# Kernel optimization log

Measured on AMD Instinct MI355X. Metric: run time of the kernel, lower is better.

## Reference

```python
import jax, jax.numpy as jnp
import numpy as np

B, N, F_IN, F_OUT = 8, 2048, 64, 64
NEG = -9.0e15  # matches torch's -9000000000000000.0 mask value


def setup_inputs() -> dict:
    key = jax.random.key(0)
    ks = jax.random.split(key, 12)
    stdv1 = 1.0 / np.sqrt(F_IN)
    stdv2 = 1.0 / np.sqrt(2 * F_OUT)
    x = jax.random.normal(ks[0], (B, N, F_IN), dtype=jnp.float32)
    adj = jax.random.randint(ks[1], (B, N, N), 0, 2).astype(jnp.int32)
    identity = jnp.broadcast_to(jnp.eye(N, dtype=jnp.int32), (B, N, N))
    def unif(k, shape, s):
        return jax.random.uniform(k, shape, jnp.float32, -s, s)
    return {
        "x": x, "adj": adj, "identity": identity,
        "W1": unif(ks[2], (F_OUT, F_IN), stdv1), "b1": unif(ks[3], (F_OUT,), stdv1),
        "a1": unif(ks[4], (1, 2 * F_OUT), stdv2), "ab1": unif(ks[5], (1,), stdv2),
        "W2": unif(ks[6], (F_OUT, F_IN), stdv1), "b2": unif(ks[7], (F_OUT,), stdv1),
        "a2": unif(ks[8], (1, 2 * F_OUT), stdv2), "ab2": unif(ks[9], (1,), stdv2),
    }


def _gat_layer(x, mask, W, b, a, ab):
    # linear1
    h = jnp.einsum('bnf,of->bno', x, W) + b                     # [B,N,Fo]
    Fo = h.shape[-1]
    # linear2 on concat(h_i, h_j) decomposes: e_ij = relu(h_i.a1 + h_j.a2 + ab)
    s1 = h @ a[0, :Fo]                                          # [B,N]
    s2 = h @ a[0, Fo:]                                          # [B,N]
    e = jax.nn.relu(s1[:, :, None] + s2[:, None, :] + ab[0])    # [B,N,N]
    e = jnp.where(mask > 0, e, NEG)
    att = jax.nn.softmax(e, axis=2)                             # [B,N,N]
    return jnp.einsum('bnm,bmf->bnf', att, h)                   # dropout p=0 / eval


def reference(x, adj, identity, W1, b1, a1, ab1, W2, b2, a2, ab2):
    out1 = _gat_layer(x, adj, W1, b1, a1, ab1)
    out2 = _gat_layer(x, identity, W2, b2, a2, ab2)
    return out1 + out2
```

## Files before the change

### kernel.cpp

```cpp
#include <hip/hip_runtime.h>


#define DEVI __device__ __forceinline__

typedef __attribute__((ext_vector_type(8))) short short8;
typedef __attribute__((ext_vector_type(4))) float floatx4;

DEVI unsigned short f2bf(float x) {
    unsigned u = __builtin_bit_cast(unsigned, x);
    unsigned r = u + 0x7FFFu + ((u >> 16) & 1u);
    return (unsigned short)(r >> 16);
}

DEVI short8 pack8(const float* v) {
    short8 r;
#pragma unroll
    for (int i = 0; i < 8; ++i) r[i] = (short)f2bf(v[i]);
    return r;
}

DEVI unsigned cvt_pk_bf16(float lo, float hi) {
    unsigned r;
    asm("v_cvt_pk_bf16_f32 %0, %1, %2" : "=v"(r) : "v"(lo), "v"(hi));
    return r;
}

DEVI void team_sync() {
    __builtin_amdgcn_sched_barrier(0);
    asm volatile("s_waitcnt lgkmcnt(0)" ::: "memory");
    __builtin_amdgcn_s_barrier();
    __builtin_amdgcn_sched_barrier(0);
}

__global__ __launch_bounds__(256) void k_prep(
    const float* __restrict__ x, const float* __restrict__ W1,
    const float* __restrict__ b1, const float* __restrict__ a1,
    const float* __restrict__ ab1,
    unsigned short* __restrict__ hT1,
    float* __restrict__ expt1,
    float* __restrict__ expv)
{
    __shared__ __align__(16) unsigned short hstage[64][72];
    const int tid = threadIdx.x;
    const int w = tid >> 6, lane = tid & 63;
    const int g = lane >> 4, r15 = lane & 15;
    const int blockRow = blockIdx.x * 64;
    const int rowbase = blockRow + w * 16;

    float xa[8], xb[8];
    const float* xrow = x + (long)(rowbase + r15) * 64;
#pragma unroll
    for (int e = 0; e < 8; ++e) { xa[e] = xrow[g * 8 + e]; xb[e] = xrow[32 + g * 8 + e]; }
    short8 A0 = pack8(xa), A1 = pack8(xb);

    floatx4 acc[4];
#pragma unroll
    for (int nt = 0; nt < 4; ++nt) {
        float wa[8], wb[8];
        const float* wrow = W1 + (nt * 16 + r15) * 64;
#pragma unroll
        for (int e = 0; e < 8; ++e) { wa[e] = wrow[g * 8 + e]; wb[e] = wrow[32 + g * 8 + e]; }
        short8 B0 = pack8(wa), B1 = pack8(wb);
        floatx4 c = {0.f, 0.f, 0.f, 0.f};
        c = __builtin_amdgcn_mfma_f32_16x16x32_bf16(A0, B0, c, 0, 0, 0);
        c = __builtin_amdgcn_mfma_f32_16x16x32_bf16(A1, B1, c, 0, 0, 0);
        float bias = b1[nt * 16 + r15];
#pragma unroll
        for (int q = 0; q < 4; ++q) c[q] += bias;
        acc[nt] = c;
    }

    float a1lo[4], a1hi[4];
#pragma unroll
    for (int nt = 0; nt < 4; ++nt) {
        a1lo[nt] = a1[nt * 16 + r15];
        a1hi[nt] = a1[64 + nt * 16 + r15];
    }
    float s1q[4], s2q[4];
#pragma unroll
    for (int q = 0; q < 4; ++q) {
        float s1 = 0.f, s2 = 0.f;
#pragma unroll
        for (int nt = 0; nt < 4; ++nt) { s1 += acc[nt][q] * a1lo[nt]; s2 += acc[nt][q] * a1hi[nt]; }
#pragma unroll
        for (int m = 1; m < 16; m <<= 1) { s1 += __shfl_xor(s1, m); s2 += __shfl_xor(s2, m); }
        s1q[q] = s1; s2q[q] = s2;
    }
    if (r15 == 0) {
        float abv = ab1[0];
#pragma unroll
        for (int q = 0; q < 4; ++q) {
            expt1[rowbase + 4 * g + q] = __expf(s1q[q] + abv);
            expv[rowbase + 4 * g + q]  = __expf(s2q[q]);
        }
    }

#pragma unroll
    for (int nt = 0; nt < 4; ++nt)
#pragma unroll
        for (int q = 0; q < 4; ++q)
            hstage[nt * 16 + r15][w * 16 + 4 * g + q] = f2bf(acc[nt][q]);
    __syncthreads();
    {
        const int o = tid >> 2, seg = (tid & 3) * 16;
        const int bb = blockRow >> 11;
        const int ib = blockRow & 2047;
        unsigned short* dst = hT1 + ((long)(bb * 64 + o) * 2048) + ib + seg;
        uint4 v0 = *(const uint4*)&hstage[o][seg];
        uint4 v1 = *(const uint4*)&hstage[o][seg + 8];
        *(uint4*)dst = v0;
        *(uint4*)(dst + 8) = v1;
    }
}

__global__ __launch_bounds__(1024, 4) void k_attn(
    const float* __restrict__ x, const int* __restrict__ adj,
    const float* __restrict__ W2, const float* __restrict__ b2,
    const unsigned short* __restrict__ hT1,
    const float* __restrict__ expt1, const float* __restrict__ expv,
    float* __restrict__ out)
{
    __shared__ __align__(16) unsigned short hl[4][2][64][72];
    __shared__ __align__(16) float vlds[2048];

    const int tid = threadIdx.x;
    const int w = tid >> 6, lane = tid & 63;
    const int t = w >> 2, wrow = w & 3;
    const int g = lane >> 4, r15 = lane & 15;
    const int bb = blockIdx.x & 7;
    const int it = blockIdx.x >> 3;
    const int rowbase = it * 64 + wrow * 16;
    const int jt0 = t * 8;

    *(float2*)&vlds[tid * 2] = *(const float2*)&expv[bb * 2048 + tid * 2];

    const float u = expt1[bb * 2048 + rowbase + r15];

    floatx4 acc[4];
#pragma unroll
    for (int nt = 0; nt < 4; ++nt) acc[nt] = (floatx4){0.f, 0.f, 0.f, 0.f};
    floatx4 acc5 = {0.f, 0.f, 0.f, 0.f};

    short8 ones;
#pragma unroll
    for (int i = 0; i < 8; ++i) ones[i] = (short)0x3F80;

    const int4* adjq = (const int4*)(adj + (long)(bb * 2048 + rowbase + r15) * 2048);

    const int ttid = tid & 255;
    const int so = ttid >> 2, sseg = (ttid & 3) * 16;
    const unsigned short* hTsrc = hT1 + (long)(bb * 64 + so) * 2048 + sseg;
    unsigned short* hldst0 = &hl[t][0][so][sseg];
    unsigned short* hldst1 = &hl[t][1][so][sseg];

    int4 adjR[2][4];
    uint4 hrg[2][2];

#define ADJ(c) do {                                                            \
        const int base_ = (jt0 + (c)) * 16 + g * 2;                            \
        adjR[(c) & 1][0] = adjq[base_];                                        \
        adjR[(c) & 1][1] = adjq[base_ + 1];                                    \
        adjR[(c) & 1][2] = adjq[base_ + 8];                                    \
        adjR[(c) & 1][3] = adjq[base_ + 9];                                    \
    } while (0)

#define HTLOAD(c) do {                                                         \
        const unsigned short* s_ = hTsrc + (jt0 + (c)) * 64;                   \
        hrg[(c) & 1][0] = *(const uint4*)s_;                                   \
        hrg[(c) & 1][1] = *(const uint4*)(s_ + 8);                             \
    } while (0)

#define HTSTORE(c) do {                                                        \
        unsigned short* d_ = ((c) & 1) ? hldst1 : hldst0;                      \
        *(uint4*)d_ = hrg[(c) & 1][0];                                         \
        *(uint4*)(d_ + 8) = hrg[(c) & 1][1];                                   \
    } while (0)

#define COMPUTE(C) do {                                                        \
        const int vb_ = (jt0 + (C)) * 64 + g * 8;                              \
        float4 v0_ = *(const float4*)&vlds[vb_];                               \
        float4 v1_ = *(const float4*)&vlds[vb_ + 4];                           \
        float4 v2_ = *(const float4*)&vlds[vb_ + 32];                          \
        float4 v3_ = *(const float4*)&vlds[vb_ + 36];                          \
        int4 j0_ = adjR[(C) & 1][0], j1_ = adjR[(C) & 1][1];                   \
        int4 j2_ = adjR[(C) & 1][2], j3_ = adjR[(C) & 1][3];                   \
        uint4 au_, bu_;                                                        \
        au_.x = cvt_pk_bf16(j0_.x > 0 ? fmaxf(u * v0_.x, 1.f) : 0.f,           \
                            j0_.y > 0 ? fmaxf(u * v0_.y, 1.f) : 0.f);          \
        au_.y = cvt_pk_bf16(j0_.z > 0 ? fmaxf(u * v0_.z, 1.f) : 0.f,           \
                            j0_.w > 0 ? fmaxf(u * v0_.w, 1.f) : 0.f);          \
        au_.z = cvt_pk_bf16(j1_.x > 0 ? fmaxf(u * v1_.x, 1.f) : 0.f,           \
                            j1_.y > 0 ? fmaxf(u * v1_.y, 1.f) : 0.f);          \
        au_.w = cvt_pk_bf16(j1_.z > 0 ? fmaxf(u * v1_.z, 1.f) : 0.f,           \
                            j1_.w > 0 ? fmaxf(u * v1_.w, 1.f) : 0.f);          \
        bu_.x = cvt_pk_bf16(j2_.x > 0 ? fmaxf(u * v2_.x, 1.f) : 0.f,           \
                            j2_.y > 0 ? fmaxf(u * v2_.y, 1.f) : 0.f);          \
        bu_.y = cvt_pk_bf16(j2_.z > 0 ? fmaxf(u * v2_.z, 1.f) : 0.f,           \
                            j2_.w > 0 ? fmaxf(u * v2_.w, 1.f) : 0.f);          \
        bu_.z = cvt_pk_bf16(j3_.x > 0 ? fmaxf(u * v3_.x, 1.f) : 0.f,           \
                            j3_.y > 0 ? fmaxf(u * v3_.y, 1.f) : 0.f);          \
        bu_.w = cvt_pk_bf16(j3_.z > 0 ? fmaxf(u * v3_.z, 1.f) : 0.f,           \
                            j3_.w > 0 ? fmaxf(u * v3_.w, 1.f) : 0.f);          \
        short8 a0 = __builtin_bit_cast(short8, au_);                           \
        short8 a1 = __builtin_bit_cast(short8, bu_);                           \
        _Pragma("unroll")                                                      \
        for (int nt_ = 0; nt_ < 4; ++nt_) {                                    \
            short8 b0 = *(const short8*)&hl[t][(C) & 1][nt_ * 16 + r15][g * 8];      \
            short8 b1 = *(const short8*)&hl[t][(C) & 1][nt_ * 16 + r15][32 + g * 8]; \
            acc[nt_] = __builtin_amdgcn_mfma_f32_16x16x32_bf16(a0, b0, acc[nt_], 0, 0, 0); \
            acc[nt_] = __builtin_amdgcn_mfma_f32_16x16x32_bf16(a1, b1, acc[nt_], 0, 0, 0); \
        }                                                                      \
        acc5 = __builtin_amdgcn_mfma_f32_16x16x32_bf16(a0, ones, acc5, 0, 0, 0); \
        acc5 = __builtin_amdgcn_mfma_f32_16x16x32_bf16(a1, ones, acc5, 0, 0, 0); \
    } while (0)

    ADJ(0); ADJ(1);
    HTLOAD(0);
    HTSTORE(0);
    HTLOAD(1);
    team_sync();

#pragma unroll
    for (int C = 0; C < 8; ++C) {
        if (C < 6) HTLOAD(C + 2);
        if (C < 7) HTSTORE(C + 1);
        COMPUTE(C);
        if (C < 6) ADJ(C + 2);
        team_sync();
    }

#undef COMPUTE
#undef HTSTORE
#undef HTLOAD
#undef ADJ

    float* csh = (float*)&hl[0][0][0][0];
    if (t > 0) {
        const int wb = ((t - 1) * 4 + wrow) * 20;
#pragma unroll
        for (int nt = 0; nt < 4; ++nt)
#pragma unroll
            for (int q = 0; q < 4; ++q)
                csh[(wb + nt * 4 + q) * 64 + lane] = acc[nt][q];
#pragma unroll
        for (int q = 0; q < 4; ++q)
            csh[(wb + 16 + q) * 64 + lane] = acc5[q];
    }
    __syncthreads();

    if (t == 0) {
#pragma unroll
        for (int ti = 0; ti < 3; ++ti) {
            const int wb = (ti * 4 + wrow) * 20;
#pragma unroll
            for (int nt = 0; nt < 4; ++nt)
#pragma unroll
                for (int q = 0; q < 4; ++q)
                    acc[nt][q] += csh[(wb + nt * 4 + q) * 64 + lane];
#pragma unroll
            for (int q = 0; q < 4; ++q)
                acc5[q] += csh[(wb + 16 + q) * 64 + lane];
        }
        float linv[4];
#pragma unroll
        for (int q = 0; q < 4; ++q) linv[q] = 1.0f / acc5[q];

        float xa[8], xb[8];
        const float* xrow = x + ((long)(bb * 2048 + rowbase + r15)) * 64;
#pragma unroll
        for (int e = 0; e < 8; ++e) { xa[e] = xrow[g * 8 + e]; xb[e] = xrow[32 + g * 8 + e]; }
        short8 A0 = pack8(xa), A1 = pack8(xb);
#pragma unroll
        for (int nt = 0; nt < 4; ++nt) {
            float wa[8], wb[8];
            const float* wrow2 = W2 + (nt * 16 + r15) * 64;
#pragma unroll
            for (int e = 0; e < 8; ++e) { wa[e] = wrow2[g * 8 + e]; wb[e] = wrow2[32 + g * 8 + e]; }
            short8 B0 = pack8(wa), B1 = pack8(wb);
            floatx4 c = {0.f, 0.f, 0.f, 0.f};
            c = __builtin_amdgcn_mfma_f32_16x16x32_bf16(A0, B0, c, 0, 0, 0);
            c = __builtin_amdgcn_mfma_f32_16x16x32_bf16(A1, B1, c, 0, 0, 0);
            float bias = b2[nt * 16 + r15];
#pragma unroll
            for (int q = 0; q < 4; ++q) {
                float val = acc[nt][q] * linv[q] + c[q] + bias;
                out[((long)(bb * 2048 + rowbase + 4 * g + q)) * 64 + nt * 16 + r15] = val;
            }
        }
    }
}

extern "C" void kernel_launch(void* const* d_in, const int* in_sizes, int n_in,
                              void* d_out, int out_size, void* d_ws, size_t ws_size,
                              hipStream_t stream) {
    const float* x   = (const float*)d_in[0];
    const int*   adj = (const int*)d_in[1];
    const float* W1  = (const float*)d_in[3];
    const float* b1  = (const float*)d_in[4];
    const float* a1  = (const float*)d_in[5];
    const float* ab1 = (const float*)d_in[6];
    const float* W2  = (const float*)d_in[7];
    const float* b2  = (const float*)d_in[8];

    unsigned short* hT1 = (unsigned short*)d_ws;
    float* expt1 = (float*)((char*)d_ws + (size_t)8 * 64 * 2048 * 2);
    float* expv  = expt1 + 8 * 2048;

    k_prep<<<256, 256, 0, stream>>>(x, W1, b1, a1, ab1, hT1, expt1, expv);
    k_attn<<<256, 1024, 0, stream>>>(x, adj, W2, b2, hT1, expt1, expv, (float*)d_out);
}
```

Before: 39.61 us.

## Halve attention block size, XOR-swizzle the hT LDS tile, and reorder staging

Each attention block now has 512 threads in four 2-wave teams, covering 32 rows. This doubles the grid to 512 blocks. The padded 72-wide LDS tile for hT is replaced by an unpadded 64-wide tile with an XOR swizzle on 16-byte chunks, to avoid bank conflicts without the padding. Global-to-register staging of hT drops from two register buffers to one: each chunk is loaded before compute and written to LDS after it. This trades some prefetch depth for fewer registers and finer work distribution, and it depends on team_sync matching the new 2-wave team size.

```diff
diff --git a/kernel.cpp b/kernel.cpp
--- a/kernel.cpp
+++ b/kernel.cpp
@@ -113,26 +113,26 @@
     }
 }
 
-__global__ __launch_bounds__(1024, 4) void k_attn(
+__global__ __launch_bounds__(512, 4) void k_attn(
     const float* __restrict__ x, const int* __restrict__ adj,
     const float* __restrict__ W2, const float* __restrict__ b2,
     const unsigned short* __restrict__ hT1,
     const float* __restrict__ expt1, const float* __restrict__ expv,
     float* __restrict__ out)
 {
-    __shared__ __align__(16) unsigned short hl[4][2][64][72];
+    __shared__ __align__(16) unsigned short hl[4][2][64][64];
     __shared__ __align__(16) float vlds[2048];
 
     const int tid = threadIdx.x;
     const int w = tid >> 6, lane = tid & 63;
-    const int t = w >> 2, wrow = w & 3;
+    const int t = w >> 1, wrow = w & 1;
     const int g = lane >> 4, r15 = lane & 15;
     const int bb = blockIdx.x & 7;
     const int it = blockIdx.x >> 3;
-    const int rowbase = it * 64 + wrow * 16;
+    const int rowbase = it * 32 + wrow * 16;
     const int jt0 = t * 8;
 
-    *(float2*)&vlds[tid * 2] = *(const float2*)&expv[bb * 2048 + tid * 2];
+    *(float4*)&vlds[tid * 4] = *(const float4*)&expv[bb * 2048 + tid * 4];
 
     const float u = expt1[bb * 2048 + rowbase + r15];
 
@@ -147,14 +147,13 @@
 
     const int4* adjq = (const int4*)(adj + (long)(bb * 2048 + rowbase + r15) * 2048);
 
-    const int ttid = tid & 255;
-    const int so = ttid >> 2, sseg = (ttid & 3) * 16;
-    const unsigned short* hTsrc = hT1 + (long)(bb * 64 + so) * 2048 + sseg;
-    unsigned short* hldst0 = &hl[t][0][so][sseg];
-    unsigned short* hldst1 = &hl[t][1][so][sseg];
+    const int ttid = tid & 127;
+    const int so = ttid >> 1, ch = ttid & 1;
+    const unsigned short* hTsrc = hT1 + (long)(bb * 64 + so) * 2048 + ch * 32;
+    unsigned short* hlw = &hl[t][0][0][0];
 
     int4 adjR[2][4];
-    uint4 hrg[2][2];
+    uint4 hrg[4];
 
 #define ADJ(c) do {                                                            \
         const int base_ = (jt0 + (c)) * 16 + g * 2;                            \
@@ -166,14 +165,17 @@
 
 #define HTLOAD(c) do {                                                         \
         const unsigned short* s_ = hTsrc + (jt0 + (c)) * 64;                   \
-        hrg[(c) & 1][0] = *(const uint4*)s_;                                   \
-        hrg[(c) & 1][1] = *(const uint4*)(s_ + 8);                             \
+        hrg[0] = *(const uint4*)s_;                                            \
+        hrg[1] = *(const uint4*)(s_ + 8);                                      \
+        hrg[2] = *(const uint4*)(s_ + 16);                                     \
+        hrg[3] = *(const uint4*)(s_ + 24);                                     \
     } while (0)
 
 #define HTSTORE(c) do {                                                        \
-        unsigned short* d_ = ((c) & 1) ? hldst1 : hldst0;                      \
-        *(uint4*)d_ = hrg[(c) & 1][0];                                         \
-        *(uint4*)(d_ + 8) = hrg[(c) & 1][1];                                   \
+        const int bo_ = ((c) & 1) * 4096 + so * 64;                            \
+        _Pragma("unroll")                                                      \
+        for (int k_ = 0; k_ < 4; ++k_)                                         \
+            *(uint4*)&hlw[bo_ + (((ch * 4 + k_) ^ (so & 7)) * 8)] = hrg[k_];   \
     } while (0)
 
 #define COMPUTE(C) do {                                                        \
@@ -203,10 +205,13 @@
                             j3_.w > 0 ? fmaxf(u * v3_.w, 1.f) : 0.f);          \
         short8 a0 = __builtin_bit_cast(short8, au_);                           \
         short8 a1 = __builtin_bit_cast(short8, bu_);                           \
+        const int bufo_ = ((C) & 1) * 4096;                                    \
+        const int sw_ = r15 & 7;                                               \
         _Pragma("unroll")                                                      \
         for (int nt_ = 0; nt_ < 4; ++nt_) {                                    \
-            short8 b0 = *(const short8*)&hl[t][(C) & 1][nt_ * 16 + r15][g * 8];      \
-            short8 b1 = *(const short8*)&hl[t][(C) & 1][nt_ * 16 + r15][32 + g * 8]; \
+            const int ro_ = bufo_ + (nt_ * 16 + r15) * 64;                     \
+            short8 b0 = *(const short8*)&hlw[ro_ + ((g ^ sw_) * 8)];           \
+            short8 b1 = *(const short8*)&hlw[ro_ + (((4 + g) ^ sw_) * 8)];     \
             acc[nt_] = __builtin_amdgcn_mfma_f32_16x16x32_bf16(a0, b0, acc[nt_], 0, 0, 0); \
             acc[nt_] = __builtin_amdgcn_mfma_f32_16x16x32_bf16(a1, b1, acc[nt_], 0, 0, 0); \
         }                                                                      \
@@ -217,14 +222,13 @@
     ADJ(0); ADJ(1);
     HTLOAD(0);
     HTSTORE(0);
-    HTLOAD(1);
     team_sync();
 
 #pragma unroll
     for (int C = 0; C < 8; ++C) {
-        if (C < 6) HTLOAD(C + 2);
+        if (C < 7) HTLOAD(C + 1);
+        COMPUTE(C);
         if (C < 7) HTSTORE(C + 1);
-        COMPUTE(C);
         if (C < 6) ADJ(C + 2);
         team_sync();
     }
@@ -236,7 +240,7 @@
 
     float* csh = (float*)&hl[0][0][0][0];
     if (t > 0) {
-        const int wb = ((t - 1) * 4 + wrow) * 20;
+        const int wb = ((t - 1) * 2 + wrow) * 20;
 #pragma unroll
         for (int nt = 0; nt < 4; ++nt)
 #pragma unroll
@@ -251,7 +255,7 @@
     if (t == 0) {
 #pragma unroll
         for (int ti = 0; ti < 3; ++ti) {
-            const int wb = (ti * 4 + wrow) * 20;
+            const int wb = (ti * 2 + wrow) * 20;
 #pragma unroll
             for (int nt = 0; nt < 4; ++nt)
 #pragma unroll
@@ -307,5 +311,5 @@
     float* expv  = expt1 + 8 * 2048;
 
     k_prep<<<256, 256, 0, stream>>>(x, W1, b1, a1, ab1, hT1, expt1, expv);
-    k_attn<<<256, 1024, 0, stream>>>(x, adj, W2, b2, hT1, expt1, expv, (float*)d_out);
-}
+    k_attn<<<512, 512, 0, stream>>>(x, adj, W2, b2, hT1, expt1, expv, (float*)d_out);
+}
```

Result: no change. 40.33 us (+1.8%).
